# Optimization experiments

Measured on AMD Instinct MI355X. Metric: run time of the kernel, lower is better.

The kernel has to match this reference:

```python
import jax, jax.numpy as jnp
import numpy as np

N_V = 40000
N_E = 640000
D_V = 128


def setup_inputs() -> dict:
    key = jax.random.key(0)
    k1, k2, k3, k4 = jax.random.split(key, 4)
    nodes = jax.random.normal(k1, (N_V, D_V), dtype=jnp.float32)
    edge_index = jax.random.randint(k2, (2, N_E), 0, N_V, dtype=jnp.int64)
    # Linear(d_v, d_v) parameters (torch default init: U(-1/sqrt(fan_in), 1/sqrt(fan_in)))
    bound = 1.0 / np.sqrt(D_V)
    W = jax.random.uniform(k3, (D_V, D_V), minval=-bound, maxval=bound, dtype=jnp.float32)
    b = jax.random.uniform(k4, (D_V,), minval=-bound, maxval=bound, dtype=jnp.float32)
    return {"nodes": nodes, "edge_index": edge_index, "W": W, "b": b}


def reference(nodes, edge_index, W, b):
    # GCN: out = act(Linear(D @ (A + I) @ D @ x)), A[src, dst] = 1,
    # deg_j = in-degree of node j (incl. self-loop), d = deg**-0.5.
    # Sparse form: (D A D x)_i = d_i * (sum_{edges (i->j)} d_j x_j + d_i x_i)
    n = nodes.shape[0]
    src, dst = edge_index[0], edge_index[1]
    deg = jax.ops.segment_sum(jnp.ones_like(dst, dtype=nodes.dtype), dst,
                              num_segments=n) + 1.0  # self-loop
    d = jax.lax.rsqrt(deg)                            # [N]
    msg = nodes[dst] * d[dst, None]                   # [E, D] gather
    agg = jax.ops.segment_sum(msg, src, num_segments=n)  # [N, D] scatter-add
    h = d[:, None] * (agg + d[:, None] * nodes)       # normalized aggregation
    return jax.nn.relu(h @ W.T + b)
```

## Files before the change

kernel.cpp:

```cpp
#include <hip/hip_runtime.h>
#include <hip/hip_fp16.h>

typedef short short8 __attribute__((ext_vector_type(8)));
typedef float floatx4 __attribute__((ext_vector_type(4)));

struct f4 { float x, y, z, w; };
struct u4v { unsigned x, y, z, w; };

#define BINW 10240
#define NB   40960
#define NBKT 2560
#define EBCAP 512
#define CAP  64
#define NCHS 128
#define NCHD 32

__device__ __forceinline__ short f2bf(float f) {
    unsigned u = __builtin_bit_cast(unsigned, f);
    u += 0x7fffu + ((u >> 16) & 1u);
    return (short)(u >> 16);
}

__global__ __launch_bounds__(1024) void k_hist(const int* __restrict__ src,
                                               const int* __restrict__ dst,
                                               unsigned* __restrict__ hist,
                                               unsigned* __restrict__ cnt_cb_t,
                                               const float* __restrict__ nodes,
                                               unsigned* __restrict__ nodes_h,
                                               const float* __restrict__ W,
                                               unsigned short* __restrict__ W_h,
                                               int ne, int nconv) {
    __shared__ unsigned bins[BINW];
    __shared__ unsigned cb[NBKT];
    if (blockIdx.x < NCHS) {
        const int c = blockIdx.x;
        for (int i = threadIdx.x; i < NBKT; i += 1024) cb[i] = 0;
        __syncthreads();
        const int csz = (ne + NCHS - 1) / NCHS;
        const int ebeg = c * csz;
        const int eend = min(ne, ebeg + csz);
        for (int e = ebeg + threadIdx.x; e < eend; e += 1024)
            atomicAdd(&cb[(unsigned)src[e] >> 4], 1u);
        __syncthreads();
        for (int i = threadIdx.x; i < NBKT; i += 1024)
            cnt_cb_t[(size_t)i * NCHS + c] = cb[i];
    } else {
        const int c = blockIdx.x - NCHS;
        for (int i = threadIdx.x; i < BINW; i += 1024) bins[i] = 0;
        __syncthreads();
        const int csz = (ne + NCHD - 1) / NCHD;
        const int ebeg = c * csz;
        const int eend = min(ne, ebeg + csz);
        for (int e = ebeg + threadIdx.x; e < eend; e += 1024) {
            const unsigned t = (unsigned)dst[e];
            atomicAdd(&bins[t >> 2], 1u << (8 * (t & 3)));
        }
        __syncthreads();
        unsigned* hp = hist + (size_t)c * BINW;
        for (int i = threadIdx.x; i < BINW; i += 1024) hp[i] = bins[i];
    }
    const int gi = blockIdx.x * 1024 + threadIdx.x;
    if (nodes_h != nullptr) {
        for (int i = gi; i < nconv; i += (NCHS + NCHD) * 1024) {
            const f4 a = ((const f4*)nodes)[(size_t)i * 2];
            const f4 b = ((const f4*)nodes)[(size_t)i * 2 + 1];
            u4v p;
            p.x = (unsigned)__half_as_ushort(__float2half(a.x)) |
                  ((unsigned)__half_as_ushort(__float2half(a.y)) << 16);
            p.y = (unsigned)__half_as_ushort(__float2half(a.z)) |
                  ((unsigned)__half_as_ushort(__float2half(a.w)) << 16);
            p.z = (unsigned)__half_as_ushort(__float2half(b.x)) |
                  ((unsigned)__half_as_ushort(__float2half(b.y)) << 16);
            p.w = (unsigned)__half_as_ushort(__float2half(b.z)) |
                  ((unsigned)__half_as_ushort(__float2half(b.w)) << 16);
            ((u4v*)nodes_h)[i] = p;
        }
    }
    if (gi < 2048) {
        const f4 a = ((const f4*)W)[(size_t)gi * 2];
        const f4 b = ((const f4*)W)[(size_t)gi * 2 + 1];
        u4v p;
        p.x = (unsigned)(unsigned short)f2bf(a.x) | ((unsigned)(unsigned short)f2bf(a.y) << 16);
        p.y = (unsigned)(unsigned short)f2bf(a.z) | ((unsigned)(unsigned short)f2bf(a.w) << 16);
        p.z = (unsigned)(unsigned short)f2bf(b.x) | ((unsigned)(unsigned short)f2bf(b.y) << 16);
        p.w = (unsigned)(unsigned short)f2bf(b.z) | ((unsigned)(unsigned short)f2bf(b.w) << 16);
        ((u4v*)W_h)[gi] = p;
    }
}

__global__ void k_scan(const unsigned* __restrict__ hist,
                       const unsigned* __restrict__ cnt_cb_t,
                       unsigned* __restrict__ cb_off_t, unsigned* __restrict__ btot,
                       float* __restrict__ d, int nv) {
    const int i = blockIdx.x * blockDim.x + threadIdx.x;
    if (i < nv) {
        const unsigned char* hd = (const unsigned char*)hist;
        int deg = 0;
#pragma unroll
        for (int c = 0; c < NCHD; ++c) deg += hd[(size_t)c * NB + i];
        d[i] = rsqrtf(1.0f + (float)deg);
    }
    if (i < NBKT) {
        unsigned acc = 0;
#pragma unroll 4
        for (int c = 0; c < NCHS; ++c) {
            cb_off_t[(size_t)i * NCHS + c] = acc;
            acc += cnt_cb_t[(size_t)i * NCHS + c];
        }
        btot[i] = acc;
    }
}

__global__ __launch_bounds__(1024) void k_fill_p1(const int* __restrict__ src,
                                                  const int* __restrict__ dst,
                                                  const unsigned* __restrict__ cb_off_t,
                                                  unsigned* __restrict__ ebuf,
                                                  int ne) {
    __shared__ unsigned cur[NBKT];
    __shared__ unsigned co[NBKT];
    const int c = blockIdx.x;
    for (int i = threadIdx.x; i < NBKT; i += 1024) {
        cur[i] = 0;
        co[i] = cb_off_t[(size_t)i * NCHS + c];
    }
    __syncthreads();
    const int csz = (ne + NCHS - 1) / NCHS;
    const int ebeg = c * csz;
    const int eend = min(ne, ebeg + csz);
    for (int e = ebeg + threadIdx.x; e < eend; e += 1024) {
        const unsigned s = (unsigned)src[e];
        const unsigned b = s >> 4;
        const unsigned pos = co[b] + atomicAdd(&cur[b], 1u);
        if (pos < EBCAP)
            ebuf[(size_t)b * EBCAP + pos] = ((s & 15u) << 16) | (unsigned)dst[e];
    }
}

__global__ __launch_bounds__(256) void k_gather_gemm(
    const float* __restrict__ nodes, const unsigned* __restrict__ nodes_h,
    const unsigned* __restrict__ ebuf, const unsigned* __restrict__ btot,
    const float* __restrict__ d, const unsigned short* __restrict__ W_h,
    const float* __restrict__ bias, float* __restrict__ out, int nv) {
    __shared__ unsigned short htile[16][136];
    __shared__ unsigned short alds[16][CAP];
    __shared__ unsigned curl[16];

    const int wave = threadIdx.x >> 6;
    const int lane = threadIdx.x & 63;
    const int q = lane >> 4;
    const int l16 = lane & 15;
    const int tile = blockIdx.x;

    if (threadIdx.x < 16) curl[threadIdx.x] = 0;
    __syncthreads();
    {
        const unsigned tot = min(btot[tile], (unsigned)EBCAP);
        const unsigned* ep = ebuf + (size_t)tile * EBCAP;
        for (unsigned k = threadIdx.x; k < tot; k += 256) {
            const unsigned u = ep[k];
            const unsigned sl = u >> 16;
            const unsigned pos = atomicAdd(&curl[sl], 1u);
            if (pos < CAP) alds[sl][pos] = (unsigned short)(u & 0xffffu);
        }
    }
    __syncthreads();

    for (int ii = 0; ii < 4; ++ii) {
        const int node = tile * 16 + wave * 4 + ii;
        const int mm = min((int)curl[wave * 4 + ii], 63);
        const int total = mm + 1;
        const int jl = (lane < mm) ? (int)alds[wave * 4 + ii][lane]
                                   : ((lane == mm) ? node : 0);
        const float wl = (lane <= mm) ? d[jl] : 0.0f;

        float acc[8];
#pragma unroll
        for (int k = 0; k < 8; ++k) acc[k] = 0.0f;

        if (nodes_h != nullptr) {
            for (int t = 0; t < total; t += 16) {
                const int j0 = __shfl(jl, t + q);
                const float w0 = __shfl(wl, t + q);
                const int j1 = __shfl(jl, t + q + 4);
                const float w1 = __shfl(wl, t + q + 4);
                const int j2 = __shfl(jl, t + q + 8);
                const float w2 = __shfl(wl, t + q + 8);
                const int j3 = __shfl(jl, t + q + 12);
                const float w3 = __shfl(wl, t + q + 12);
                const u4v h0 = ((const u4v*)nodes_h)[(size_t)j0 * 16 + l16];
                const u4v h1 = ((const u4v*)nodes_h)[(size_t)j1 * 16 + l16];
                const u4v h2 = ((const u4v*)nodes_h)[(size_t)j2 * 16 + l16];
                const u4v h3 = ((const u4v*)nodes_h)[(size_t)j3 * 16 + l16];
                const __half2* p0 = (const __half2*)&h0;
                const __half2* p1 = (const __half2*)&h1;
                const __half2* p2 = (const __half2*)&h2;
                const __half2* p3 = (const __half2*)&h3;
#pragma unroll
                for (int k = 0; k < 4; ++k) {
                    float2 f;
                    f = __half22float2(p0[k]); acc[2*k] += w0 * f.x; acc[2*k+1] += w0 * f.y;
                    f = __half22float2(p1[k]); acc[2*k] += w1 * f.x; acc[2*k+1] += w1 * f.y;
                    f = __half22float2(p2[k]); acc[2*k] += w2 * f.x; acc[2*k+1] += w2 * f.y;
                    f = __half22float2(p3[k]); acc[2*k] += w3 * f.x; acc[2*k+1] += w3 * f.y;
                }
            }
        } else {
            for (int t = 0; t < total; t += 4) {
                const int tt = t + q;
                const int j = __shfl(jl, tt);
                const float w = __shfl(wl, tt);
                const f4 v0 = *(const f4*)(nodes + (size_t)j * 128 + l16 * 8);
                const f4 v1 = *(const f4*)(nodes + (size_t)j * 128 + l16 * 8 + 4);
                acc[0] += w * v0.x; acc[1] += w * v0.y; acc[2] += w * v0.z; acc[3] += w * v0.w;
                acc[4] += w * v1.x; acc[5] += w * v1.y; acc[6] += w * v1.z; acc[7] += w * v1.w;
            }
        }

#pragma unroll
        for (int k = 0; k < 8; ++k) {
            acc[k] += __shfl_xor(acc[k], 16);
            acc[k] += __shfl_xor(acc[k], 32);
        }

        if (q == 0) {
            const float di = d[node];
            float hv[8];
#pragma unroll
            for (int k = 0; k < 8; ++k) hv[k] = di * acc[k];
            u4v p;
            p.x = (unsigned)(unsigned short)f2bf(hv[0]) | ((unsigned)(unsigned short)f2bf(hv[1]) << 16);
            p.y = (unsigned)(unsigned short)f2bf(hv[2]) | ((unsigned)(unsigned short)f2bf(hv[3]) << 16);
            p.z = (unsigned)(unsigned short)f2bf(hv[4]) | ((unsigned)(unsigned short)f2bf(hv[5]) << 16);
            p.w = (unsigned)(unsigned short)f2bf(hv[6]) | ((unsigned)(unsigned short)f2bf(hv[7]) << 16);
            *(u4v*)&htile[wave * 4 + ii][l16 * 8] = p;
        }
    }

    __syncthreads();

    const int l15 = lane & 15;
    const int lhi = lane >> 4;

    short8 Af[4];
#pragma unroll
    for (int kt = 0; kt < 4; ++kt)
        Af[kt] = *(const short8*)&htile[l15][kt * 32 + lhi * 8];

#pragma unroll
    for (int n2 = 0; n2 < 2; ++n2) {
        const int nt = wave * 2 + n2;
        const float bv = bias[nt * 16 + l15];
        floatx4 acc = {0.f, 0.f, 0.f, 0.f};
#pragma unroll
        for (int kt = 0; kt < 4; ++kt) {
            const short8 Bf = *(const short8*)(W_h + (size_t)(nt * 16 + l15) * 128 + kt * 32 + lhi * 8);
            acc = __builtin_amdgcn_mfma_f32_16x16x32_bf16(Af[kt], Bf, acc, 0, 0, 0);
        }
#pragma unroll
        for (int r = 0; r < 4; ++r) {
            const int row = tile * 16 + lhi * 4 + r;
            if (row < nv)
                out[(size_t)row * 128 + nt * 16 + l15] = fmaxf(acc[r] + bv, 0.0f);
        }
    }
}

extern "C" void kernel_launch(void* const* d_in, const int* in_sizes, int n_in,
                              void* d_out, int out_size, void* d_ws, size_t ws_size,
                              hipStream_t stream) {
    const float* nodes = (const float*)d_in[0];
    const int*   ei    = (const int*)d_in[1];
    const float* W     = (const float*)d_in[2];
    const float* bias  = (const float*)d_in[3];
    float* out = (float*)d_out;

    const int NV = in_sizes[0] / 128;
    const int NE = in_sizes[1] / 2;
    const int* src = ei;
    const int* dst = ei + NE;

    const size_t words = ws_size / 4;
    const size_t base_w = (size_t)NCHD * BINW + (size_t)2 * NBKT * NCHS + NBKT +
                          (size_t)NB + 8192 + (size_t)NBKT * EBCAP;
    const bool use_fp16 = (base_w + (size_t)NB * 64) <= words;

    unsigned* p = (unsigned*)d_ws;
    unsigned* hist     = p;                     p += (size_t)NCHD * BINW;
    unsigned* cnt_cb_t = p;                     p += (size_t)NBKT * NCHS;
    unsigned* cb_off_t = p;                     p += (size_t)NBKT * NCHS;
    unsigned* btot     = p;                     p += NBKT;
    float*    d        = (float*)p;             p += NB;
    unsigned short* W_h = (unsigned short*)p;   p += 8192;
    unsigned* ebuf     = p;                     p += (size_t)NBKT * EBCAP;
    unsigned* nodes_h  = use_fp16 ? p : nullptr;

    const int nconv = NV * 16;
    k_hist<<<NCHS + NCHD, 1024, 0, stream>>>(src, dst, hist, cnt_cb_t,
                                             nodes, nodes_h, W, W_h, NE, nconv);

    const int nthreads = max(NV, NBKT);
    k_scan<<<(nthreads + 255) / 256, 256, 0, stream>>>(
        hist, cnt_cb_t, cb_off_t, btot, d, NV);

    k_fill_p1<<<NCHS, 1024, 0, stream>>>(src, dst, cb_off_t, ebuf, NE);

    const int ntiles = (NV + 15) / 16;
    k_gather_gemm<<<ntiles, 256, 0, stream>>>(nodes, nodes_h, ebuf, btot, d,
                                              W_h, bias, out, NV);
}
```

Baseline: 81.64 us.

## Merge histogram, scan and fill kernels into one cooperative kernel with grid syncs

Folds the histogram, scan and bucket-fill phases into a single cooperative kernel of 160 blocks. The phases are separated by grid-wide syncs and the shared-memory arrays are reused across phases. The goal is to remove two kernel launches and the idle gaps between them. If the cooperative launch fails, the code falls back to three separate kernels. In exchange it adds grid-sync cost and cooperative launch overhead, and the scan phase now runs on 1024-thread blocks.

```diff
diff --git a/kernel.cpp b/kernel.cpp
--- a/kernel.cpp
+++ b/kernel.cpp
@@ -1,5 +1,8 @@
 #include <hip/hip_runtime.h>
 #include <hip/hip_fp16.h>
+#include <hip/hip_cooperative_groups.h>
+
+namespace cg = cooperative_groups;
 
 typedef short short8 __attribute__((ext_vector_type(8)));
 typedef float floatx4 __attribute__((ext_vector_type(4)));
@@ -14,6 +17,7 @@
 #define CAP  64
 #define NCHS 128
 #define NCHD 32
+#define NBLD (NCHS + NCHD)
 
 __device__ __forceinline__ short f2bf(float f) {
     unsigned u = __builtin_bit_cast(unsigned, f);
@@ -21,17 +25,16 @@
     return (short)(u >> 16);
 }
 
-__global__ __launch_bounds__(1024) void k_hist(const int* __restrict__ src,
-                                               const int* __restrict__ dst,
-                                               unsigned* __restrict__ hist,
-                                               unsigned* __restrict__ cnt_cb_t,
-                                               const float* __restrict__ nodes,
-                                               unsigned* __restrict__ nodes_h,
-                                               const float* __restrict__ W,
-                                               unsigned short* __restrict__ W_h,
-                                               int ne, int nconv) {
-    __shared__ unsigned bins[BINW];
-    __shared__ unsigned cb[NBKT];
+__device__ __forceinline__ void phaseA(unsigned* bins, unsigned* cb,
+                                       const int* __restrict__ src,
+                                       const int* __restrict__ dst,
+                                       unsigned* __restrict__ hist,
+                                       unsigned* __restrict__ cnt_cb_t,
+                                       const float* __restrict__ nodes,
+                                       unsigned* __restrict__ nodes_h,
+                                       const float* __restrict__ W,
+                                       unsigned short* __restrict__ W_h,
+                                       int ne, int nconv) {
     if (blockIdx.x < NCHS) {
         const int c = blockIdx.x;
         for (int i = threadIdx.x; i < NBKT; i += 1024) cb[i] = 0;
@@ -44,7 +47,7 @@
         __syncthreads();
         for (int i = threadIdx.x; i < NBKT; i += 1024)
             cnt_cb_t[(size_t)i * NCHS + c] = cb[i];
-    } else {
+    } else if (blockIdx.x < NBLD) {
         const int c = blockIdx.x - NCHS;
         for (int i = threadIdx.x; i < BINW; i += 1024) bins[i] = 0;
         __syncthreads();
@@ -61,7 +64,7 @@
     }
     const int gi = blockIdx.x * 1024 + threadIdx.x;
     if (nodes_h != nullptr) {
-        for (int i = gi; i < nconv; i += (NCHS + NCHD) * 1024) {
+        for (int i = gi; i < nconv; i += NBLD * 1024) {
             const f4 a = ((const f4*)nodes)[(size_t)i * 2];
             const f4 b = ((const f4*)nodes)[(size_t)i * 2 + 1];
             u4v p;
@@ -88,11 +91,12 @@
     }
 }
 
-__global__ void k_scan(const unsigned* __restrict__ hist,
-                       const unsigned* __restrict__ cnt_cb_t,
-                       unsigned* __restrict__ cb_off_t, unsigned* __restrict__ btot,
-                       float* __restrict__ d, int nv) {
-    const int i = blockIdx.x * blockDim.x + threadIdx.x;
+__device__ __forceinline__ void phaseB(const unsigned* __restrict__ hist,
+                                       const unsigned* __restrict__ cnt_cb_t,
+                                       unsigned* __restrict__ cb_off_t,
+                                       unsigned* __restrict__ btot,
+                                       float* __restrict__ d, int nv) {
+    const int i = blockIdx.x * 1024 + threadIdx.x;
     if (i < nv) {
         const unsigned char* hd = (const unsigned char*)hist;
         int deg = 0;
@@ -111,13 +115,12 @@
     }
 }
 
-__global__ __launch_bounds__(1024) void k_fill_p1(const int* __restrict__ src,
-                                                  const int* __restrict__ dst,
-                                                  const unsigned* __restrict__ cb_off_t,
-                                                  unsigned* __restrict__ ebuf,
-                                                  int ne) {
-    __shared__ unsigned cur[NBKT];
-    __shared__ unsigned co[NBKT];
+__device__ __forceinline__ void phaseC(unsigned* cur, unsigned* co,
+                                       const int* __restrict__ src,
+                                       const int* __restrict__ dst,
+                                       const unsigned* __restrict__ cb_off_t,
+                                       unsigned* __restrict__ ebuf, int ne) {
+    if (blockIdx.x >= NCHS) return;
     const int c = blockIdx.x;
     for (int i = threadIdx.x; i < NBKT; i += 1024) {
         cur[i] = 0;
@@ -134,6 +137,44 @@
         if (pos < EBCAP)
             ebuf[(size_t)b * EBCAP + pos] = ((s & 15u) << 16) | (unsigned)dst[e];
     }
+}
+
+__global__ __launch_bounds__(1024) void k_build(
+    const int* src, const int* dst, unsigned* hist, unsigned* cnt_cb_t,
+    unsigned* cb_off_t, unsigned* btot, float* d, const float* nodes,
+    unsigned* nodes_h, const float* W, unsigned short* W_h, unsigned* ebuf,
+    int ne, int nv, int nconv) {
+    cg::grid_group grid = cg::this_grid();
+    __shared__ unsigned bins[BINW];
+    __shared__ unsigned cb[NBKT];
+    phaseA(bins, cb, src, dst, hist, cnt_cb_t, nodes, nodes_h, W, W_h, ne, nconv);
+    grid.sync();
+    phaseB(hist, cnt_cb_t, cb_off_t, btot, d, nv);
+    grid.sync();
+    phaseC(cb, bins, src, dst, cb_off_t, ebuf, ne);
+}
+
+__global__ __launch_bounds__(1024) void kA(const int* src, const int* dst,
+                                           unsigned* hist, unsigned* cnt_cb_t,
+                                           const float* nodes, unsigned* nodes_h,
+                                           const float* W, unsigned short* W_h,
+                                           int ne, int nconv) {
+    __shared__ unsigned bins[BINW];
+    __shared__ unsigned cb[NBKT];
+    phaseA(bins, cb, src, dst, hist, cnt_cb_t, nodes, nodes_h, W, W_h, ne, nconv);
+}
+__global__ __launch_bounds__(1024) void kB(const unsigned* hist,
+                                           const unsigned* cnt_cb_t,
+                                           unsigned* cb_off_t, unsigned* btot,
+                                           float* d, int nv) {
+    phaseB(hist, cnt_cb_t, cb_off_t, btot, d, nv);
+}
+__global__ __launch_bounds__(1024) void kC(const int* src, const int* dst,
+                                           const unsigned* cb_off_t,
+                                           unsigned* ebuf, int ne) {
+    __shared__ unsigned cur[NBKT];
+    __shared__ unsigned co[NBKT];
+    phaseC(cur, co, src, dst, cb_off_t, ebuf, ne);
 }
 
 __global__ __launch_bounds__(256) void k_gather_gemm(
@@ -294,15 +335,25 @@
     unsigned* ebuf     = p;                     p += (size_t)NBKT * EBCAP;
     unsigned* nodes_h  = use_fp16 ? p : nullptr;
 
-    const int nconv = NV * 16;
-    k_hist<<<NCHS + NCHD, 1024, 0, stream>>>(src, dst, hist, cnt_cb_t,
-                                             nodes, nodes_h, W, W_h, NE, nconv);
-
-    const int nthreads = max(NV, NBKT);
-    k_scan<<<(nthreads + 255) / 256, 256, 0, stream>>>(
-        hist, cnt_cb_t, cb_off_t, btot, d, NV);
-
-    k_fill_p1<<<NCHS, 1024, 0, stream>>>(src, dst, cb_off_t, ebuf, NE);
+    int ne_ = NE, nv_ = NV, nconv_ = NV * 16;
+    const int* src_ = src;
+    const int* dst_ = dst;
+    const float* nodes_ = nodes;
+    const float* W_ = W;
+    void* args[] = { (void*)&src_, (void*)&dst_, (void*)&hist, (void*)&cnt_cb_t,
+                     (void*)&cb_off_t, (void*)&btot, (void*)&d, (void*)&nodes_,
+                     (void*)&nodes_h, (void*)&W_, (void*)&W_h, (void*)&ebuf,
+                     (void*)&ne_, (void*)&nv_, (void*)&nconv_ };
+    hipError_t err = hipLaunchCooperativeKernel((const void*)k_build,
+                                                dim3(NBLD), dim3(1024),
+                                                args, 0, stream);
+    if (err != hipSuccess) {
+        kA<<<NBLD, 1024, 0, stream>>>(src, dst, hist, cnt_cb_t, nodes, nodes_h,
+                                      W, W_h, NE, nconv_);
+        kB<<<(max(NV, NBKT) + 1023) / 1024, 1024, 0, stream>>>(
+            hist, cnt_cb_t, cb_off_t, btot, d, NV);
+        kC<<<NCHS, 1024, 0, stream>>>(src, dst, cb_off_t, ebuf, NE);
+    }
 
     const int ntiles = (NV + 15) / 16;
     k_gather_gemm<<<ntiles, 256, 0, stream>>>(nodes, nodes_h, ebuf, btot, d,
```

New measurement: 174.1 us. 2.13x slower.
